# Optimization experiments

Measured on AMD Instinct MI355X. Metric: run time of the kernel, lower is better.

The kernel has to match this reference:

```python
import jax, jax.numpy as jnp
import numpy as np

B, T, D = 2, 2048, 1024
H, RANK = 16, 16
HD = D // H  # 64


def setup_inputs() -> dict:
    key = jax.random.key(0)
    ks = jax.random.split(key, 10)
    x = jax.random.normal(ks[0], (B, T, D), dtype=jnp.float32)
    def lin(k):
        kw, kb = jax.random.split(k)
        W = jax.random.normal(kw, (D, D), dtype=jnp.float32) * (1.0 / np.sqrt(D))
        b = jax.random.normal(kb, (D,), dtype=jnp.float32) * 0.01
        return W, b
    Wq, bq = lin(ks[1])
    Wk, bk = lin(ks[2])
    Wv, bv = lin(ks[3])
    Wo, bo = lin(ks[4])
    # per-head low-rank metric factors A_h: (min(rank, head_dim), head_dim)
    A = jax.random.normal(ks[5], (H, min(RANK, HD), HD), dtype=jnp.float32) * 0.02
    log_lambda = jnp.full((H,), jnp.log(jnp.float32(0.1)), dtype=jnp.float32)
    return {"x": x, "Wq": Wq, "bq": bq, "Wk": Wk, "bk": bk,
            "Wv": Wv, "bv": bv, "Wo": Wo, "bo": bo,
            "A": A, "log_lambda": log_lambda}


def reference(x, Wq, bq, Wk, bk, Wv, bv, Wo, bo, A, log_lambda):
    b, t, d = x.shape
    h = A.shape[0]
    hd = d // h

    def split_heads(y):
        return y.reshape(b, t, h, hd).transpose(0, 2, 1, 3)  # (b,h,t,hd)

    q = split_heads(x @ Wq.T + bq)
    k = split_heads(x @ Wk.T + bk)
    v = split_heads(x @ Wv.T + bv)

    # Metric g_h = A_h^T A_h + lam_h * I. torch.einsum('btid,dd,btjd->btj')
    # uses only diag(g) and sums over i: dist[b,t,j] = sum_d S[b,t,d]*gdiag[d]*diff[b,t,j,d]
    # where S[b,t,d] = sum_i (q[b,t,d] - k[b,i,d]) = t*q - sum_i k.
    gdiag = jnp.sum(A * A, axis=1) + jnp.exp(log_lambda)[:, None]  # (h,hd)

    ksum = jnp.sum(k, axis=2)                      # (b,h,hd)
    S = jnp.float32(t) * q - ksum[:, :, None, :]   # (b,h,t,hd)
    Sg = S * gdiag[None, :, None, :]               # (b,h,t,hd)
    c = jnp.sum(Sg * q, axis=-1)                   # (b,h,t)
    # dist_sq[b,h,t,j] = c[b,h,t] - sum_d Sg[b,h,t,d] * k[b,h,j,d]
    dist_sq = c[..., None] - jnp.einsum('bhtd,bhjd->bhtj', Sg, k)
    attn = jax.nn.softmax(-dist_sq, axis=-1)       # (b,h,t,t)
    o = jnp.einsum('bhtj,bhjd->bhtd', attn, v)     # (b,h,t,hd)
    out = o.transpose(0, 2, 1, 3).reshape(b, t, d)
    return out @ Wo.T + bo
```

## Files before the change

### kernel.cpp

```cpp
#include <hip/hip_runtime.h>
#include <math.h>

#define D_MODEL 1024
#define NHEAD   16
#define HDIM    64
#define SEQ     2048
#define BATCH   2
#define NROWS   (BATCH*SEQ)

typedef unsigned short u16;
typedef __attribute__((ext_vector_type(4))) unsigned short u16x4;
typedef __attribute__((ext_vector_type(8))) short short8;
typedef __attribute__((ext_vector_type(4))) float f32x4;
typedef __attribute__((ext_vector_type(2))) unsigned int u32x2;

#define SWZ(row, c) (((c) ^ ((row) & 7)) * 8)
#define GF(row) ((((row) + ((row) >> 2))) & 3)

__device__ __forceinline__ u16 f2bf(float x) {
    unsigned int u = __float_as_uint(x);
    u += 0x7fffu + ((u >> 16) & 1u);
    return (u16)(u >> 16);
}
__device__ __forceinline__ float bf2f(u16 h) {
    return __uint_as_float(((unsigned int)h) << 16);
}
__device__ __forceinline__ unsigned int cvt_pk_bf16(float a, float b) {
    unsigned int r;
    asm("v_cvt_pk_bf16_f32 %0, %1, %2" : "=v"(r) : "v"(a), "v"(b));
    return r;
}
__device__ __forceinline__ void st8(u16* p, short8 v) {
    u16x4 a, b;
    a[0]=(u16)v[0]; a[1]=(u16)v[1]; a[2]=(u16)v[2]; a[3]=(u16)v[3];
    b[0]=(u16)v[4]; b[1]=(u16)v[5]; b[2]=(u16)v[6]; b[3]=(u16)v[7];
    *(u16x4*)p = a; *(u16x4*)(p + 4) = b;
}
__device__ __forceinline__ void gld16(const u16* g, u16* l) {
    __builtin_amdgcn_global_load_lds(
        (const __attribute__((address_space(1))) void*)g,
        (__attribute__((address_space(3))) void*)l, 16, 0, 0);
}

__device__ __forceinline__ void xcd_decode(int bid, int& member, int& g) {
    const int xcd = bid & 7;
    const int rest = bid >> 3;
    member = rest & 15;
    g = ((rest >> 4) << 3) | xcd;
}

__global__ void gdiag_kernel(const float* __restrict__ A,
                             const float* __restrict__ log_lambda,
                             float* __restrict__ gdiag) {
    int id = blockIdx.x * 256 + threadIdx.x;
    if (id >= NHEAD * HDIM) return;
    int h = id >> 6, d = id & 63;
    float s = 0.f;
#pragma unroll
    for (int i = 0; i < 16; ++i) {
        float a = A[(h * 16 + i) * HDIM + d];
        s += a * a;
    }
    gdiag[id] = (s + __expf(log_lambda[h])) * 1.4426950408889634f;
}

__global__ void prep_split(const float* __restrict__ x,
                           const float* __restrict__ Wq, const float* __restrict__ Wk,
                           const float* __restrict__ Wv, const float* __restrict__ Wo,
                           u16* __restrict__ xh, u16* __restrict__ xl,
                           u16* __restrict__ wqh, u16* __restrict__ wql,
                           u16* __restrict__ wkh, u16* __restrict__ wkl,
                           u16* __restrict__ wvh, u16* __restrict__ woh) {
    int seg = blockIdx.y;
    int i = blockIdx.x * 256 + threadIdx.x;
    const float* src; u16* dh; u16* dl; int n4;
    if      (seg == 0) { src = x;  dh = xh;  dl = xl;      n4 = NROWS * D_MODEL / 4; }
    else if (seg == 1) { src = Wq; dh = wqh; dl = wql;     n4 = D_MODEL * D_MODEL / 4; }
    else if (seg == 2) { src = Wk; dh = wkh; dl = wkl;     n4 = D_MODEL * D_MODEL / 4; }
    else if (seg == 3) { src = Wv; dh = wvh; dl = nullptr; n4 = D_MODEL * D_MODEL / 4; }
    else               { src = Wo; dh = woh; dl = nullptr; n4 = D_MODEL * D_MODEL / 4; }
    if (i >= n4) return;
    float4 v = *(const float4*)&src[(size_t)i * 4];
    float vv[4] = {v.x, v.y, v.z, v.w};
    u16x4 hv, lv;
#pragma unroll
    for (int j = 0; j < 4; ++j) {
        u16 hb = f2bf(vv[j]);
        hv[j] = hb;
        lv[j] = f2bf(vv[j] - bf2f(hb));
    }
    *(u16x4*)&dh[(size_t)i * 4] = hv;
    if (dl) *(u16x4*)&dl[(size_t)i * 4] = lv;
}

template<int NP3>
__global__ __launch_bounds__(512, 4)
void gemm_mfma(const u16* __restrict__ Ah, const u16* __restrict__ Al,
               const u16* __restrict__ BhA, const u16* __restrict__ BlA, const float* __restrict__ biasA,
               float* outfA, u16* auxhA, u16* auxlA, float* ksumA,
               const u16* __restrict__ BhB, const u16* __restrict__ BlB, const float* __restrict__ biasB,
               float* outfB, u16* auxhB, u16* auxlB, float* ksumB,
               int out_layout) {
    int xtile, g;
    xcd_decode(blockIdx.x, xtile, g);
    const int ytile = g & 31;
    const int z = g >> 5;

    const u16* Bh = (z == 0) ? BhA : BhB;
    const u16* Bl = (z == 0) ? BlA : BlB;
    const float* bias = (z == 0) ? biasA : biasB;
    float* outf = (z == 0) ? outfA : outfB;
    u16* auxh   = (z == 0) ? auxhA : auxhB;
    u16* auxl   = (z == 0) ? auxlA : auxlB;
    float* ksump= (z == 0) ? ksumA : ksumB;

    __shared__ __align__(16) u16 As_h[128][32], Bs_h[64][32];
    __shared__ __align__(16) u16 As_l[NP3 ? 128 : 1][32], Bs_l[NP3 ? 64 : 1][32];

    const int tid = threadIdx.x;
    const int w = tid >> 6, lane = tid & 63, quad = lane >> 4, n16 = lane & 15;
    const int rBase = ytile * 128;
    const int cBase = xtile * 64;

    const int lrow = lane >> 2;
    const int lch  = lane & 3;
    const int arow = w * 16 + lrow;
    const int asc  = ((lch ^ GF(arow)) * 8);
    const int brow = (w & 3) * 16 + lrow;
    const int bsc  = ((lch ^ GF(brow)) * 8);

    f32x4 acc[4] = {};

    for (int kt = 0; kt < D_MODEL; kt += 32) {
        gld16(&Ah[(size_t)(rBase + arow) * D_MODEL + kt + asc], &As_h[w * 16][0]);
        if (NP3) gld16(&Al[(size_t)(rBase + arow) * D_MODEL + kt + asc], &As_l[w * 16][0]);
        if (w < 4) {
            gld16(&Bh[(size_t)(cBase + brow) * D_MODEL + kt + bsc], &Bs_h[(w & 3) * 16][0]);
        } else if (NP3) {
            gld16(&Bl[(size_t)(cBase + brow) * D_MODEL + kt + bsc], &Bs_l[NP3 ? (w & 3) * 16 : 0][0]);
        }
        __syncthreads();

        short8 a_h, a_l;
        {
            const int row = w * 16 + n16;
            const int cc = (quad ^ GF(row)) * 8;
            a_h = *(const short8*)&As_h[row][cc];
            if (NP3) a_l = *(const short8*)&As_l[NP3 ? row : 0][cc];
        }
#pragma unroll
        for (int nt = 0; nt < 4; ++nt) {
            const int row = nt * 16 + n16;
            const int cc = (quad ^ GF(row)) * 8;
            short8 b_h = *(const short8*)&Bs_h[row][cc];
            short8 b_l;
            if (NP3) b_l = *(const short8*)&Bs_l[NP3 ? row : 0][cc];
            acc[nt] = __builtin_amdgcn_mfma_f32_16x16x32_bf16(a_h, b_h, acc[nt], 0, 0, 0);
            if (NP3) {
                acc[nt] = __builtin_amdgcn_mfma_f32_16x16x32_bf16(a_h, b_l, acc[nt], 0, 0, 0);
                acc[nt] = __builtin_amdgcn_mfma_f32_16x16x32_bf16(a_l, b_h, acc[nt], 0, 0, 0);
            }
        }
        __syncthreads();
    }

    float csum[4];
#pragma unroll
    for (int nt = 0; nt < 4; ++nt) csum[nt] = 0.f;
#pragma unroll
    for (int nt = 0; nt < 4; ++nt) {
        int c = cBase + nt * 16 + n16;
        float bc = bias[c];
        int rb = rBase + w * 16 + quad * 4;
#pragma unroll
        for (int reg = 0; reg < 4; ++reg) {
            float val = acc[nt][reg] + bc;
            int rr = rb + reg;
            size_t idx = out_layout
                ? ((size_t)(((rr >> 11) * NHEAD + (c >> 6)) * SEQ + (rr & (SEQ - 1)))) * HDIM + (c & 63)
                : (size_t)rr * D_MODEL + c;
            if (outf) outf[idx] = val;
            if (auxh) {
                u16 hb = f2bf(val);
                auxh[idx] = hb;
                if (auxl) auxl[idx] = f2bf(val - bf2f(hb));
            }
            csum[nt] += val;
        }
    }
    if (ksump) {
#pragma unroll
        for (int nt = 0; nt < 4; ++nt) {
            float cs = csum[nt];
            cs += __shfl_xor(cs, 16);
            cs += __shfl_xor(cs, 32);
            if (quad == 0) {
                int c = cBase + nt * 16 + n16;
                int bb = rBase >> 11;
                atomicAdd(&ksump[(bb * NHEAD + (c >> 6)) * HDIM + (c & 63)], cs);
            }
        }
    }
}

__global__ __launch_bounds__(256)
void vtrans_kernel(const u16* __restrict__ vh, u16* __restrict__ vT) {
    __shared__ u16 tile[64][72];
    const int tid = threadIdx.x;
    const int t0 = blockIdx.x * 64;
    const int bh = blockIdx.y;
    const u16* vp = vh + (size_t)bh * SEQ * HDIM;
#pragma unroll
    for (int s = 0; s < 2; ++s) {
        int id = s * 256 + tid;
        int row = id >> 3, c8 = (id & 7) * 8;
        st8(&tile[row][c8], *(const short8*)&vp[(size_t)(t0 + row) * HDIM + c8]);
    }
    __syncthreads();
#pragma unroll
    for (int s = 0; s < 2; ++s) {
        int id = s * 256 + tid;
        int d = id >> 3, t8 = (id & 7) * 8;
        short8 r;
#pragma unroll
        for (int i = 0; i < 8; ++i) r[i] = (short)tile[t8 + i][d];
        *(short8*)&vT[((size_t)bh * HDIM + d) * SEQ + t0 + t8] = r;
    }
}

__device__ __forceinline__ void qk_mfma(f32x4 (&lg)[2][4],
                                        const u16 (*kh)[64], const u16 (*kl)[64],
                                        const short8 (&sgh)[2][2], const short8 (&sgl)[2][2],
                                        int quad, int n16) {
#pragma unroll
    for (int mt = 0; mt < 2; ++mt)
#pragma unroll
        for (int nt = 0; nt < 4; ++nt) lg[mt][nt] = (f32x4){0.f, 0.f, 0.f, 0.f};
#pragma unroll
    for (int kc = 0; kc < 2; ++kc) {
#pragma unroll
        for (int nt = 0; nt < 4; ++nt) {
            const int row = nt * 16 + n16;
            const int cc = SWZ(row, kc * 4 + quad);
            short8 b_h = *(const short8*)&kh[row][cc];
            short8 b_l = *(const short8*)&kl[row][cc];
#pragma unroll
            for (int mt = 0; mt < 2; ++mt) {
                lg[mt][nt] = __builtin_amdgcn_mfma_f32_16x16x32_bf16(b_h, sgh[mt][kc], lg[mt][nt], 0, 0, 0);
                lg[mt][nt] = __builtin_amdgcn_mfma_f32_16x16x32_bf16(b_l, sgh[mt][kc], lg[mt][nt], 0, 0, 0);
                lg[mt][nt] = __builtin_amdgcn_mfma_f32_16x16x32_bf16(b_h, sgl[mt][kc], lg[mt][nt], 0, 0, 0);
            }
        }
    }
}

__device__ __forceinline__ void softmax_pv(f32x4 (&lg)[2][4], float (&m_n)[2], float (&l_n)[2],
                                           f32x4 (&oaccv)[2][4],
                                           u16 (*psw)[64],
                                           const u16 (*vt)[64],
                                           int quad, int n16) {
    float mx[2];
#pragma unroll
    for (int mt = 0; mt < 2; ++mt) {
        float m0 = fmaxf(fmaxf(lg[mt][0][0], lg[mt][0][1]), lg[mt][0][2]);
        m0 = fmaxf(fmaxf(m0, lg[mt][0][3]), lg[mt][1][0]);
        m0 = fmaxf(fmaxf(m0, lg[mt][1][1]), lg[mt][1][2]);
        m0 = fmaxf(fmaxf(m0, lg[mt][1][3]), lg[mt][2][0]);
        m0 = fmaxf(fmaxf(m0, lg[mt][2][1]), lg[mt][2][2]);
        m0 = fmaxf(fmaxf(m0, lg[mt][2][3]), lg[mt][3][0]);
        m0 = fmaxf(fmaxf(m0, lg[mt][3][1]), lg[mt][3][2]);
        m0 = fmaxf(m0, lg[mt][3][3]);
        m0 = fmaxf(m0, __shfl_xor(m0, 16));
        mx[mt] = fmaxf(m0, __shfl_xor(m0, 32));
    }
    const float need = fmaxf(mx[0] - m_n[0], mx[1] - m_n[1]);
    if (!__all(need <= 8.f)) {
#pragma unroll
        for (int mt = 0; mt < 2; ++mt) {
            const float mn = fmaxf(m_n[mt], mx[mt]);
            const float alpha = exp2f(m_n[mt] - mn);
            m_n[mt] = mn;
            l_n[mt] *= alpha;
            const float a0 = __shfl(alpha, quad * 4 + 0);
            const float a1 = __shfl(alpha, quad * 4 + 1);
            const float a2 = __shfl(alpha, quad * 4 + 2);
            const float a3 = __shfl(alpha, quad * 4 + 3);
#pragma unroll
            for (int nt = 0; nt < 4; ++nt) {
                oaccv[mt][nt][0] *= a0; oaccv[mt][nt][1] *= a1;
                oaccv[mt][nt][2] *= a2; oaccv[mt][nt][3] *= a3;
            }
        }
    }
#pragma unroll
    for (int mt = 0; mt < 2; ++mt) {
        const int prow = mt * 16 + n16;
        const float mn = m_n[mt];
        float psum = 0.f;
#pragma unroll
        for (int nt = 0; nt < 4; ++nt) {
#pragma unroll
            for (int r = 0; r < 4; ++r) lg[mt][nt][r] = exp2f(lg[mt][nt][r] - mn);
            u32x2 pk;
            pk[0] = cvt_pk_bf16(lg[mt][nt][0], lg[mt][nt][1]);
            pk[1] = cvt_pk_bf16(lg[mt][nt][2], lg[mt][nt][3]);
            *(u32x2*)&psw[prow][SWZ(prow, nt * 2 + (quad >> 1)) + (quad & 1) * 4] = pk;
            psum += (lg[mt][nt][0] + lg[mt][nt][1]) + (lg[mt][nt][2] + lg[mt][nt][3]);
        }
        l_n[mt] += psum;
    }
    short8 pa[2][2];
#pragma unroll
    for (int mt = 0; mt < 2; ++mt) {
        const int prow = mt * 16 + n16;
        pa[mt][0] = *(const short8*)&psw[prow][SWZ(prow, quad)];
        pa[mt][1] = *(const short8*)&psw[prow][SWZ(prow, quad + 4)];
    }
#pragma unroll
    for (int nt = 0; nt < 4; ++nt) {
        const int row = nt * 16 + n16;
        short8 v0 = *(const short8*)&vt[row][SWZ(row, quad)];
        short8 v1 = *(const short8*)&vt[row][SWZ(row, quad + 4)];
#pragma unroll
        for (int mt = 0; mt < 2; ++mt) {
            oaccv[mt][nt] = __builtin_amdgcn_mfma_f32_16x16x32_bf16(pa[mt][0], v0, oaccv[mt][nt], 0, 0, 0);
            oaccv[mt][nt] = __builtin_amdgcn_mfma_f32_16x16x32_bf16(pa[mt][1], v1, oaccv[mt][nt], 0, 0, 0);
        }
    }
}

__global__ __launch_bounds__(256, 2)
void flash_mfma(const float* __restrict__ q, const u16* __restrict__ kh,
                const u16* __restrict__ kl, const u16* __restrict__ vT,
                const float* __restrict__ ksum, const float* __restrict__ gdiag,
                u16* __restrict__ o) {
    __shared__ __align__(16) u16 khs[2][64][64], kls[2][64][64], vTs[3][64][64];
    __shared__ __align__(16) u16 ps[4][32][64];

    const int tid = threadIdx.x;
    const int w = tid >> 6, lane = tid & 63, quad = lane >> 4, n16 = lane & 15;
    int qblk, g;
    xcd_decode(blockIdx.x, qblk, g);
    const int t0 = qblk * 128;
    const int h = g & 15, b = g >> 4;
    const size_t bh = (size_t)b * NHEAD + h;
    const float* qp = q + bh * SEQ * HDIM;
    const u16* khp = kh + bh * SEQ * HDIM;
    const u16* klp = kl + bh * SEQ * HDIM;
    const u16* vtp = vT + bh * HDIM * SEQ;

    short8 sgh[2][2], sgl[2][2];
#pragma unroll
    for (int mt = 0; mt < 2; ++mt) {
        int qrow = t0 + w * 32 + mt * 16 + n16;
#pragma unroll
        for (int kc = 0; kc < 2; ++kc) {
            int d0 = kc * 32 + quad * 8;
            float4 q0 = *(const float4*)&qp[(size_t)qrow * HDIM + d0];
            float4 q1 = *(const float4*)&qp[(size_t)qrow * HDIM + d0 + 4];
            float4 k0 = *(const float4*)&ksum[bh * HDIM + d0];
            float4 k1 = *(const float4*)&ksum[bh * HDIM + d0 + 4];
            float4 g0 = *(const float4*)&gdiag[(size_t)h * HDIM + d0];
            float4 g1 = *(const float4*)&gdiag[(size_t)h * HDIM + d0 + 4];
            float sg[8];
            sg[0] = (2048.f * q0.x - k0.x) * g0.x; sg[1] = (2048.f * q0.y - k0.y) * g0.y;
            sg[2] = (2048.f * q0.z - k0.z) * g0.z; sg[3] = (2048.f * q0.w - k0.w) * g0.w;
            sg[4] = (2048.f * q1.x - k1.x) * g1.x; sg[5] = (2048.f * q1.y - k1.y) * g1.y;
            sg[6] = (2048.f * q1.z - k1.z) * g1.z; sg[7] = (2048.f * q1.w - k1.w) * g1.w;
#pragma unroll
            for (int j = 0; j < 8; ++j) {
                u16 hb = f2bf(sg[j]);
                sgh[mt][kc][j] = (short)hb;
                sgl[mt][kc][j] = (short)f2bf(sg[j] - bf2f(hb));
            }
        }
    }

    f32x4 oaccv[2][4] = {};
    f32x4 lgP[2][4];
    float m_n[2] = {-INFINITY, -INFINITY};
    float l_n[2] = {0.f, 0.f};

    const int srow = tid >> 3;
    const int sc   = tid & 7;
    const int scg  = sc * 8;
    const int scl  = SWZ(srow, sc);

    const int NT = SEQ / 64;

    *(short8*)&khs[0][srow][scl]      = *(const short8*)&khp[(size_t)srow * HDIM + scg];
    *(short8*)&khs[0][srow + 32][scl] = *(const short8*)&khp[(size_t)(srow + 32) * HDIM + scg];
    *(short8*)&kls[0][srow][scl]      = *(const short8*)&klp[(size_t)srow * HDIM + scg];
    *(short8*)&kls[0][srow + 32][scl] = *(const short8*)&klp[(size_t)(srow + 32) * HDIM + scg];
    *(short8*)&vTs[0][srow][scl]      = *(const short8*)&vtp[(size_t)srow * SEQ + scg];
    *(short8*)&vTs[0][srow + 32][scl] = *(const short8*)&vtp[(size_t)(srow + 32) * SEQ + scg];
    __syncthreads();

    qk_mfma(lgP, khs[0], kls[0], sgh, sgl, quad, n16);
    {
        const int j0 = 64;
        *(short8*)&khs[1][srow][scl]      = *(const short8*)&khp[(size_t)(j0 + srow) * HDIM + scg];
        *(short8*)&khs[1][srow + 32][scl] = *(const short8*)&khp[(size_t)(j0 + srow + 32) * HDIM + scg];
        *(short8*)&kls[1][srow][scl]      = *(const short8*)&klp[(size_t)(j0 + srow) * HDIM + scg];
        *(short8*)&kls[1][srow + 32][scl] = *(const short8*)&klp[(size_t)(j0 + srow + 32) * HDIM + scg];
        *(short8*)&vTs[1][srow][scl]      = *(const short8*)&vtp[(size_t)srow * SEQ + j0 + scg];
        *(short8*)&vTs[1][srow + 32][scl] = *(const short8*)&vtp[(size_t)(srow + 32) * SEQ + j0 + scg];
    }

    for (int j = 1; j < NT; ++j) {
        __syncthreads();
        const int kcur = j & 1;
        const int vprev = (j - 1) % 3;
        const bool pf = (j + 1 < NT);

        short8 rk0h, rk1h, rk0l, rk1l, rv0, rv1;
        if (pf) {
            const int jn = (j + 1) * 64;
            rk0h = *(const short8*)&khp[(size_t)(jn + srow) * HDIM + scg];
            rk1h = *(const short8*)&khp[(size_t)(jn + srow + 32) * HDIM + scg];
            rk0l = *(const short8*)&klp[(size_t)(jn + srow) * HDIM + scg];
            rk1l = *(const short8*)&klp[(size_t)(jn + srow + 32) * HDIM + scg];
            rv0  = *(const short8*)&vtp[(size_t)srow * SEQ + jn + scg];
            rv1  = *(const short8*)&vtp[(size_t)(srow + 32) * SEQ + jn + scg];
        }

        f32x4 lgC[2][4];
        qk_mfma(lgC, khs[kcur], kls[kcur], sgh, sgl, quad, n16);
        softmax_pv(lgP, m_n, l_n, oaccv, ps[w], vTs[vprev], quad, n16);

        if (pf) {
            const int kn = (j + 1) & 1;
            const int vn = (j + 1) % 3;
            *(short8*)&khs[kn][srow][scl] = rk0h;  *(short8*)&khs[kn][srow + 32][scl] = rk1h;
            *(short8*)&kls[kn][srow][scl] = rk0l;  *(short8*)&kls[kn][srow + 32][scl] = rk1l;
            *(short8*)&vTs[vn][srow][scl] = rv0;   *(short8*)&vTs[vn][srow + 32][scl] = rv1;
        }

#pragma unroll
        for (int mt = 0; mt < 2; ++mt)
#pragma unroll
            for (int nt = 0; nt < 4; ++nt) lgP[mt][nt] = lgC[mt][nt];
    }

    softmax_pv(lgP, m_n, l_n, oaccv, ps[w], vTs[(NT - 1) % 3], quad, n16);

#pragma unroll
    for (int mt = 0; mt < 2; ++mt) {
        float l = l_n[mt];
        l += __shfl_xor(l, 16);
        l += __shfl_xor(l, 32);
        l_n[mt] = l;
    }
#pragma unroll
    for (int mt = 0; mt < 2; ++mt) {
#pragma unroll
        for (int r = 0; r < 4; ++r) {
            float lr = __shfl(l_n[mt], quad * 4 + r);
            float inv = 1.f / lr;
            int t = t0 + w * 32 + mt * 16 + quad * 4 + r;
#pragma unroll
            for (int nt = 0; nt < 4; ++nt) {
                int d = nt * 16 + n16;
                o[((size_t)(b * SEQ + t)) * D_MODEL + h * HDIM + d] = f2bf(oaccv[mt][nt][r] * inv);
            }
        }
    }
}

extern "C" void kernel_launch(void* const* d_in, const int* in_sizes, int n_in,
                              void* d_out, int out_size, void* d_ws, size_t ws_size,
                              hipStream_t stream) {
    const float* x  = (const float*)d_in[0];
    const float* Wq = (const float*)d_in[1];
    const float* bq = (const float*)d_in[2];
    const float* Wk = (const float*)d_in[3];
    const float* bk = (const float*)d_in[4];
    const float* Wv = (const float*)d_in[5];
    const float* bv = (const float*)d_in[6];
    const float* Wo = (const float*)d_in[7];
    const float* bo = (const float*)d_in[8];
    const float* A  = (const float*)d_in[9];
    const float* ll = (const float*)d_in[10];
    float* out = (float*)d_out;

    const size_t NQKV = (size_t)NROWS * D_MODEL;
    const size_t NW = (size_t)D_MODEL * D_MODEL;
    char* base = (char*)d_ws;
    float* q_ws = (float*)base;            base += NQKV * 4;
    u16* xh  = (u16*)base;                 base += NQKV * 2;
    u16* xl  = (u16*)base;                 base += NQKV * 2;
    u16* khw = (u16*)base;                 base += NQKV * 2;
    u16* klw = (u16*)base;                 base += NQKV * 2;
    u16* vhw = (u16*)base;                 base += NQKV * 2;
    u16* wqh = (u16*)base;                 base += NW * 2;
    u16* wql = (u16*)base;                 base += NW * 2;
    u16* wkh = (u16*)base;                 base += NW * 2;
    u16* wkl = (u16*)base;                 base += NW * 2;
    u16* wvh = (u16*)base;                 base += NW * 2;
    u16* woh = (u16*)base;                 base += NW * 2;
    float* gd_ws   = (float*)base;         base += NHEAD * HDIM * 4;
    float* ksum_ws = (float*)base;         base += BATCH * NHEAD * HDIM * 4;

    hipMemsetAsync(ksum_ws, 0, BATCH * NHEAD * HDIM * sizeof(float), stream);

    prep_split<<<dim3(4096, 5), 256, 0, stream>>>(x, Wq, Wk, Wv, Wo,
                                                  xh, xl, wqh, wql, wkh, wkl, wvh, woh);
    gdiag_kernel<<<4, 256, 0, stream>>>(A, ll, gd_ws);

    gemm_mfma<1><<<1024, 512, 0, stream>>>(
        xh, xl,
        wqh, wql, bq, q_ws, nullptr, nullptr, nullptr,
        wkh, wkl, bk, nullptr, khw, klw, ksum_ws,
        1);
    gemm_mfma<0><<<512, 512, 0, stream>>>(
        xh, nullptr,
        wvh, nullptr, bv, nullptr, vhw, nullptr, nullptr,
        wvh, nullptr, bv, nullptr, vhw, nullptr, nullptr,
        1);

    u16* vTw = xl;
    u16* ohw = xh;
    vtrans_kernel<<<dim3(SEQ / 64, BATCH * NHEAD), 256, 0, stream>>>(vhw, vTw);

    flash_mfma<<<512, 256, 0, stream>>>(
        q_ws, khw, klw, vTw, ksum_ws, gd_ws, ohw);

    gemm_mfma<0><<<512, 512, 0, stream>>>(
        ohw, nullptr,
        woh, nullptr, bo, out, nullptr, nullptr, nullptr,
        woh, nullptr, bo, out, nullptr, nullptr, nullptr,
        0);
}
```

Measured before the change: 298.5 us.

## Fuse V projection into QK GEMM launch and write V transposed directly

Merges the separate V-projection GEMM into the Q/K GEMM launch as a third z-slice, and has its epilogue write bf16 V directly in the transposed (b,h,d,t) layout. This removes the standalone transpose kernel and one kernel launch, and saves a round trip of V through memory. In exchange, the template parameter becomes a runtime flag, so the inner loop carries a runtime branch and the lo-part shared memory is always allocated, which may lower occupancy for the non-split GEMMs. The transposed stores are 4-element strided writes and may be poorly coalesced.

New measurement: 289.6 us, median of 2. 3.0% less time.

```diff
diff --git a/kernel.cpp b/kernel.cpp
--- a/kernel.cpp
+++ b/kernel.cpp
@@ -29,12 +29,6 @@
     unsigned int r;
     asm("v_cvt_pk_bf16_f32 %0, %1, %2" : "=v"(r) : "v"(a), "v"(b));
     return r;
-}
-__device__ __forceinline__ void st8(u16* p, short8 v) {
-    u16x4 a, b;
-    a[0]=(u16)v[0]; a[1]=(u16)v[1]; a[2]=(u16)v[2]; a[3]=(u16)v[3];
-    b[0]=(u16)v[4]; b[1]=(u16)v[5]; b[2]=(u16)v[6]; b[3]=(u16)v[7];
-    *(u16x4*)p = a; *(u16x4*)(p + 4) = b;
 }
 __device__ __forceinline__ void gld16(const u16* g, u16* l) {
     __builtin_amdgcn_global_load_lds(
@@ -93,29 +87,31 @@
     if (dl) *(u16x4*)&dl[(size_t)i * 4] = lv;
 }
 
-template<int NP3>
 __global__ __launch_bounds__(512, 4)
 void gemm_mfma(const u16* __restrict__ Ah, const u16* __restrict__ Al,
-               const u16* __restrict__ BhA, const u16* __restrict__ BlA, const float* __restrict__ biasA,
-               float* outfA, u16* auxhA, u16* auxlA, float* ksumA,
-               const u16* __restrict__ BhB, const u16* __restrict__ BlB, const float* __restrict__ biasB,
-               float* outfB, u16* auxhB, u16* auxlB, float* ksumB,
-               int out_layout) {
+               const u16* __restrict__ Bh0, const u16* __restrict__ Bl0, const float* __restrict__ bias0,
+               float* outf0, u16* auxh0, u16* auxl0, float* ksum0,
+               const u16* __restrict__ Bh1, const u16* __restrict__ Bl1, const float* __restrict__ bias1,
+               float* outf1, u16* auxh1, u16* auxl1, float* ksum1,
+               const u16* __restrict__ Bh2, const float* __restrict__ bias2, u16* __restrict__ auxh2,
+               int np3_mask, int layouts) {
     int xtile, g;
     xcd_decode(blockIdx.x, xtile, g);
     const int ytile = g & 31;
     const int z = g >> 5;
 
-    const u16* Bh = (z == 0) ? BhA : BhB;
-    const u16* Bl = (z == 0) ? BlA : BlB;
-    const float* bias = (z == 0) ? biasA : biasB;
-    float* outf = (z == 0) ? outfA : outfB;
-    u16* auxh   = (z == 0) ? auxhA : auxhB;
-    u16* auxl   = (z == 0) ? auxlA : auxlB;
-    float* ksump= (z == 0) ? ksumA : ksumB;
+    const u16* Bh = (z == 0) ? Bh0 : (z == 1) ? Bh1 : Bh2;
+    const u16* Bl = (z == 0) ? Bl0 : (z == 1) ? Bl1 : nullptr;
+    const float* bias = (z == 0) ? bias0 : (z == 1) ? bias1 : bias2;
+    float* outf = (z == 0) ? outf0 : (z == 1) ? outf1 : nullptr;
+    u16* auxh   = (z == 0) ? auxh0 : (z == 1) ? auxh1 : auxh2;
+    u16* auxl   = (z == 0) ? auxl0 : (z == 1) ? auxl1 : nullptr;
+    float* ksump= (z == 0) ? ksum0 : (z == 1) ? ksum1 : nullptr;
+    const bool np3 = (np3_mask >> z) & 1;
+    const int layout = (layouts >> (4 * z)) & 15;
 
     __shared__ __align__(16) u16 As_h[128][32], Bs_h[64][32];
-    __shared__ __align__(16) u16 As_l[NP3 ? 128 : 1][32], Bs_l[NP3 ? 64 : 1][32];
+    __shared__ __align__(16) u16 As_l[128][32], Bs_l[64][32];
 
     const int tid = threadIdx.x;
     const int w = tid >> 6, lane = tid & 63, quad = lane >> 4, n16 = lane & 15;
@@ -133,11 +129,11 @@
 
     for (int kt = 0; kt < D_MODEL; kt += 32) {
         gld16(&Ah[(size_t)(rBase + arow) * D_MODEL + kt + asc], &As_h[w * 16][0]);
-        if (NP3) gld16(&Al[(size_t)(rBase + arow) * D_MODEL + kt + asc], &As_l[w * 16][0]);
+        if (np3) gld16(&Al[(size_t)(rBase + arow) * D_MODEL + kt + asc], &As_l[w * 16][0]);
         if (w < 4) {
             gld16(&Bh[(size_t)(cBase + brow) * D_MODEL + kt + bsc], &Bs_h[(w & 3) * 16][0]);
-        } else if (NP3) {
-            gld16(&Bl[(size_t)(cBase + brow) * D_MODEL + kt + bsc], &Bs_l[NP3 ? (w & 3) * 16 : 0][0]);
+        } else if (np3) {
+            gld16(&Bl[(size_t)(cBase + brow) * D_MODEL + kt + bsc], &Bs_l[(w & 3) * 16][0]);
         }
         __syncthreads();
 
@@ -146,22 +142,36 @@
             const int row = w * 16 + n16;
             const int cc = (quad ^ GF(row)) * 8;
             a_h = *(const short8*)&As_h[row][cc];
-            if (NP3) a_l = *(const short8*)&As_l[NP3 ? row : 0][cc];
+            if (np3) a_l = *(const short8*)&As_l[row][cc];
         }
 #pragma unroll
         for (int nt = 0; nt < 4; ++nt) {
             const int row = nt * 16 + n16;
             const int cc = (quad ^ GF(row)) * 8;
             short8 b_h = *(const short8*)&Bs_h[row][cc];
-            short8 b_l;
-            if (NP3) b_l = *(const short8*)&Bs_l[NP3 ? row : 0][cc];
             acc[nt] = __builtin_amdgcn_mfma_f32_16x16x32_bf16(a_h, b_h, acc[nt], 0, 0, 0);
-            if (NP3) {
+            if (np3) {
+                short8 b_l = *(const short8*)&Bs_l[row][cc];
                 acc[nt] = __builtin_amdgcn_mfma_f32_16x16x32_bf16(a_h, b_l, acc[nt], 0, 0, 0);
                 acc[nt] = __builtin_amdgcn_mfma_f32_16x16x32_bf16(a_l, b_h, acc[nt], 0, 0, 0);
             }
         }
         __syncthreads();
+    }
+
+    if (layout == 2) {
+#pragma unroll
+        for (int nt = 0; nt < 4; ++nt) {
+            const int c = cBase + nt * 16 + n16;
+            const float bc = bias[c];
+            const int rb = rBase + w * 16 + quad * 4;
+            const int b = rb >> 11, t = rb & (SEQ - 1);
+            u16x4 tv;
+#pragma unroll
+            for (int reg = 0; reg < 4; ++reg) tv[reg] = f2bf(acc[nt][reg] + bc);
+            *(u16x4*)&auxh[(((size_t)b * NHEAD + (c >> 6)) * HDIM + (c & 63)) * SEQ + t] = tv;
+        }
+        return;
     }
 
     float csum[4];
@@ -176,7 +186,7 @@
         for (int reg = 0; reg < 4; ++reg) {
             float val = acc[nt][reg] + bc;
             int rr = rb + reg;
-            size_t idx = out_layout
+            size_t idx = (layout == 1)
                 ? ((size_t)(((rr >> 11) * NHEAD + (c >> 6)) * SEQ + (rr & (SEQ - 1)))) * HDIM + (c & 63)
                 : (size_t)rr * D_MODEL + c;
             if (outf) outf[idx] = val;
@@ -200,31 +210,6 @@
                 atomicAdd(&ksump[(bb * NHEAD + (c >> 6)) * HDIM + (c & 63)], cs);
             }
         }
-    }
-}
-
-__global__ __launch_bounds__(256)
-void vtrans_kernel(const u16* __restrict__ vh, u16* __restrict__ vT) {
-    __shared__ u16 tile[64][72];
-    const int tid = threadIdx.x;
-    const int t0 = blockIdx.x * 64;
-    const int bh = blockIdx.y;
-    const u16* vp = vh + (size_t)bh * SEQ * HDIM;
-#pragma unroll
-    for (int s = 0; s < 2; ++s) {
-        int id = s * 256 + tid;
-        int row = id >> 3, c8 = (id & 7) * 8;
-        st8(&tile[row][c8], *(const short8*)&vp[(size_t)(t0 + row) * HDIM + c8]);
-    }
-    __syncthreads();
-#pragma unroll
-    for (int s = 0; s < 2; ++s) {
-        int id = s * 256 + tid;
-        int d = id >> 3, t8 = (id & 7) * 8;
-        short8 r;
-#pragma unroll
-        for (int i = 0; i < 8; ++i) r[i] = (short)tile[t8 + i][d];
-        *(short8*)&vT[((size_t)bh * HDIM + d) * SEQ + t0 + t8] = r;
     }
 }
 
@@ -491,7 +476,7 @@
     u16* xl  = (u16*)base;                 base += NQKV * 2;
     u16* khw = (u16*)base;                 base += NQKV * 2;
     u16* klw = (u16*)base;                 base += NQKV * 2;
-    u16* vhw = (u16*)base;                 base += NQKV * 2;
+    u16* vTw = (u16*)base;                 base += NQKV * 2;
     u16* wqh = (u16*)base;                 base += NW * 2;
     u16* wql = (u16*)base;                 base += NW * 2;
     u16* wkh = (u16*)base;                 base += NW * 2;
@@ -507,27 +492,21 @@
                                                   xh, xl, wqh, wql, wkh, wkl, wvh, woh);
     gdiag_kernel<<<4, 256, 0, stream>>>(A, ll, gd_ws);
 
-    gemm_mfma<1><<<1024, 512, 0, stream>>>(
+    gemm_mfma<<<1536, 512, 0, stream>>>(
         xh, xl,
         wqh, wql, bq, q_ws, nullptr, nullptr, nullptr,
         wkh, wkl, bk, nullptr, khw, klw, ksum_ws,
-        1);
-    gemm_mfma<0><<<512, 512, 0, stream>>>(
-        xh, nullptr,
-        wvh, nullptr, bv, nullptr, vhw, nullptr, nullptr,
-        wvh, nullptr, bv, nullptr, vhw, nullptr, nullptr,
-        1);
-
-    u16* vTw = xl;
+        wvh, bv, vTw,
+        0b011, (1) | (1 << 4) | (2 << 8));
+
     u16* ohw = xh;
-    vtrans_kernel<<<dim3(SEQ / 64, BATCH * NHEAD), 256, 0, stream>>>(vhw, vTw);
-
     flash_mfma<<<512, 256, 0, stream>>>(
         q_ws, khw, klw, vTw, ksum_ws, gd_ws, ohw);
 
-    gemm_mfma<0><<<512, 512, 0, stream>>>(
+    gemm_mfma<<<512, 512, 0, stream>>>(
         ohw, nullptr,
         woh, nullptr, bo, out, nullptr, nullptr, nullptr,
         woh, nullptr, bo, out, nullptr, nullptr, nullptr,
-        0);
-}
+        woh, bo, nullptr,
+        0, 0);
+}
```
